# Kernel optimization log

Hardware: AMD Instinct MI355X
Metric: run time of the kernel (lower is better)

## Reference

```python
import jax, jax.numpy as jnp
import numpy as np

V = 100000   # nodes
E = 1600000  # edges (avg degree 16)
LN = 64      # feat_dim
S = 8        # stat_dim
T = 4        # recurrence steps
MU = 0.9
N_EDGE_TYPES = 10


def _uniform_linear(kw, kb, fan_out, fan_in):
    # torch nn.Linear default init: U(-1/sqrt(fan_in), 1/sqrt(fan_in))
    lim = 1.0 / np.sqrt(fan_in)
    W = jax.random.uniform(kw, (fan_out, fan_in), jnp.float32, -lim, lim)
    b = jax.random.uniform(kb, (fan_out,), jnp.float32, -lim, lim)
    return W, b


def setup_inputs() -> dict:
    key = jax.random.key(0)
    ks = jax.random.split(key, 12)
    feat_Matrix = jax.random.normal(ks[0], (V, LN), jnp.float32)
    X_Node = jax.random.randint(ks[1], (E,), 1, V + 1, dtype=jnp.int64)   # 1-indexed
    X_Neis = jax.random.randint(ks[2], (E,), 1, V + 1, dtype=jnp.int64)   # 1-indexed
    edge_type_index = jax.random.randint(ks[3], (E,), 1, N_EDGE_TYPES + 1, dtype=jnp.int32)
    dg_list = jax.random.randint(ks[4], (E,), 1, 65).astype(jnp.float32)  # degrees >= 1
    H_init = jax.random.uniform(ks[5], (V, S), jnp.float32)  # torch.rand init of state
    W_xi, b_xi = _uniform_linear(ks[6], ks[7], S * S, 2 * LN + N_EDGE_TYPES)
    W_rou, b_rou = _uniform_linear(ks[8], ks[9], S, LN)
    W1, b1 = _uniform_linear(ks[10], ks[11], 1, S)
    return {
        "feat_Matrix": feat_Matrix, "X_Node": X_Node, "X_Neis": X_Neis,
        "edge_type_index": edge_type_index, "dg_list": dg_list, "H_init": H_init,
        "W_xi": W_xi, "b_xi": b_xi, "W_rou": W_rou, "b_rou": b_rou,
        "W1": W1, "b1": b1,
    }


def reference(feat_Matrix, X_Node, X_Neis, edge_type_index, dg_list, H_init,
              W_xi, b_xi, W_rou, b_rou, W1, b1):
    src = X_Node - 1           # 0-indexed source nodes
    dst = X_Neis - 1           # 0-indexed neighbor nodes (for embedding gather)
    node_emb = feat_Matrix[src]            # [E, LN]
    neis_emb = feat_Matrix[dst]            # [E, LN]
    et = jax.nn.one_hot(edge_type_index - 1, N_EDGE_TYPES, dtype=jnp.float32)
    X = jnp.concatenate([node_emb, neis_emb, et], axis=1)  # [E, 2*LN+10]

    # Xi(X): per-edge transition matrices A, constant across steps -> precompute
    A = jnp.tanh(X @ W_xi.T + b_xi).reshape(-1, S, S)
    A = A * (MU / S) / dg_list[:, None, None]              # [E, S, S]
    # Rou(neis_emb): per-edge bias b, constant across steps
    bias = jnp.tanh(neis_emb @ W_rou.T + b_rou)            # [E, S]

    def step(H, _):
        He = H[src]                                        # gather [E, S]
        out = jnp.einsum('eij,ej->ei', A, He) + bias       # per-edge small matmul
        # AggrSum: dense one-hot mask vs RAW 1-indexed X_Neis against range(0,V-1)
        # -> scatter by 1-indexed ids; ids == V fall out of range and are dropped.
        Hn = jax.ops.segment_sum(out, X_Neis, num_segments=V)
        return Hn, None

    H, _ = jax.lax.scan(step, H_init, None, length=T)      # [V, S]

    logits = (H @ W1.T + b1).squeeze(-1)                   # [V]
    attn = jax.nn.softmax(logits)                          # softmax over nodes
    graph_out = jnp.tanh(jnp.sum(H * attn[:, None], axis=0))  # [S]
    return graph_out
```

## Files before the change

kernel.cpp:

```cpp
#include <hip/hip_runtime.h>
#include <hip/hip_bf16.h>

constexpr int V   = 100000;
constexpr int E   = 1600000;
constexpr int NET = 10;
constexpr int KXW = 138;
constexpr int NB  = (V + 255) / 256;
constexpr int GN  = 8;
constexpr float MUS   = 0.1125f;
constexpr float SP    = 0.025f;
constexpr float LOG2E = 1.44269504f;
constexpr float S2L   = 2.0f * SP * LOG2E;
constexpr float K7    = MUS / 7.0f;

typedef __attribute__((ext_vector_type(8))) short short8;
typedef __attribute__((ext_vector_type(4))) float float4v;

__device__ __forceinline__ float fast_tanh(float x) {
    return 1.0f - 2.0f * __builtin_amdgcn_rcpf(__expf(2.0f * x) + 1.0f);
}
__device__ __forceinline__ float bflo(unsigned u) { return __uint_as_float(u << 16); }
__device__ __forceinline__ float bfhi(unsigned u) { return __uint_as_float(u & 0xffff0000u); }
__device__ __forceinline__ short f2bf(float x) {
    union { __hip_bfloat16 b; short s; } u; u.b = __float2bfloat16(x); return u.s;
}

__device__ __forceinline__ float ub0(unsigned u) {
#if __has_builtin(__builtin_amdgcn_cvt_f32_ubyte0)
    return __builtin_amdgcn_cvt_f32_ubyte0(u);
#else
    return (float)(u & 0xff);
#endif
}
__device__ __forceinline__ float ub1(unsigned u) {
#if __has_builtin(__builtin_amdgcn_cvt_f32_ubyte1)
    return __builtin_amdgcn_cvt_f32_ubyte1(u);
#else
    return (float)((u >> 8) & 0xff);
#endif
}
__device__ __forceinline__ float ub2(unsigned u) {
#if __has_builtin(__builtin_amdgcn_cvt_f32_ubyte2)
    return __builtin_amdgcn_cvt_f32_ubyte2(u);
#else
    return (float)((u >> 16) & 0xff);
#endif
}
__device__ __forceinline__ float ub3(unsigned u) {
#if __has_builtin(__builtin_amdgcn_cvt_f32_ubyte3)
    return __builtin_amdgcn_cvt_f32_ubyte3(u);
#else
    return (float)(u >> 24);
#endif
}

__device__ __forceinline__ int dot8i4(unsigned a, unsigned b, int c) {
#if __has_builtin(__builtin_amdgcn_sdot8)
    return __builtin_amdgcn_sdot8((int)a, (int)b, c, false);
#else
    int r = c;
    #pragma unroll
    for (int j = 0; j < 8; ++j) {
        int av = ((int)(a << (28 - 4 * j))) >> 28;
        int bv = ((int)(b << (28 - 4 * j))) >> 28;
        r += av * bv;
    }
    return r;
#endif
}

__global__ __launch_bounds__(256) void histg_kernel(
    const int* __restrict__ xneis, int* __restrict__ countg,
    int* __restrict__ rank0)
{
    int e = blockIdx.x * 256 + threadIdx.x;
    if (e >= E) return;
    int g = blockIdx.x & (GN - 1);
    int nr = xneis[e];
    if (nr < V) rank0[e] = atomicAdd(&countg[g * V + nr], 1);
}

__global__ __launch_bounds__(256) void scanV_kernel(
    const int* __restrict__ countg, int* __restrict__ offg,
    int* __restrict__ cnt_tot, int* __restrict__ scanned, int* __restrict__ bsum)
{
    __shared__ int s[256];
    int tid = threadIdx.x;
    int i = blockIdx.x * 256 + tid;
    int c = 0;
    if (i < V) {
        int run = 0;
        #pragma unroll
        for (int g = 0; g < GN; ++g) {
            offg[g * V + i] = run;
            run += countg[g * V + i];
        }
        cnt_tot[i] = run;
        c = run;
    }
    s[tid] = c; __syncthreads();
    #pragma unroll
    for (int off = 1; off < 256; off <<= 1) {
        int t = (tid >= off) ? s[tid - off] : 0;
        __syncthreads();
        s[tid] += t;
        __syncthreads();
    }
    if (i < V) scanned[i] = s[tid] - c;
    if (tid == 255) bsum[blockIdx.x] = s[255];
}

__global__ __launch_bounds__(512) void scan_tops_kernel(
    const int* __restrict__ blocksum, int* __restrict__ tops, int* __restrict__ rowptr)
{
    __shared__ int s[512];
    int tid = threadIdx.x;
    int v = (tid < NB) ? blocksum[tid] : 0;
    s[tid] = v; __syncthreads();
    #pragma unroll
    for (int off = 1; off < 512; off <<= 1) {
        int t = (tid >= off) ? s[tid - off] : 0;
        __syncthreads();
        s[tid] += t;
        __syncthreads();
    }
    if (tid < NB) tops[tid] = s[tid] - v;
    if (tid == 511) rowptr[V] = s[511];
}

__global__ __launch_bounds__(256) void add_offsets_kernel(
    const int* __restrict__ scanned, const int* __restrict__ tops, int* __restrict__ rowptr)
{
    int i = blockIdx.x * 256 + threadIdx.x;
    if (i < V) rowptr[i] = scanned[i] + tops[blockIdx.x];
}

__global__ __launch_bounds__(256) void scatter_kernel(
    const int* __restrict__ xnode, const int* __restrict__ xneis,
    const int* __restrict__ etype, const float* __restrict__ dg,
    const int* __restrict__ rowptr, const int* __restrict__ offg,
    const int* __restrict__ rank0, unsigned* __restrict__ pmeta)
{
    int e = blockIdx.x * 256 + threadIdx.x;
    if (e >= E) return;
    int g = blockIdx.x & (GN - 1);
    int nr = xneis[e];
    if (nr < V) {
        int p = rowptr[nr] + offg[g * V + nr] + rank0[e];
        unsigned src = (unsigned)(xnode[e] - 1);
        unsigned et  = (unsigned)(etype[e] - 1);
        unsigned dgi = (unsigned)dg[e] - 1;
        pmeta[p] = src | (et << 17) | (dgi << 21);
    }
}

__global__ __launch_bounds__(256) void bsum_kernel(
    const float* __restrict__ feat, const int* __restrict__ count,
    const float* __restrict__ Wrou, const float* __restrict__ brou,
    const float* __restrict__ Hinit, float* __restrict__ Bsum,
    uint2* __restrict__ Hq0)
{
    __shared__ float Wl[512];
    __shared__ float bl[8];
    int tid = threadIdx.x;
    for (int i = tid; i < 512; i += 256) Wl[i] = Wrou[i];
    if (tid < 8) bl[tid] = brou[tid];
    __syncthreads();

    int v = blockIdx.x * 256 + tid;
    if (v >= V) return;
    int c = count[v];
    float out[8] = {0, 0, 0, 0, 0, 0, 0, 0};
    if (c > 0) {
        const float4* f4 = (const float4*)(feat + (size_t)(v - 1) * 64);
        float acc[8];
        #pragma unroll
        for (int s = 0; s < 8; ++s) acc[s] = bl[s];
        #pragma unroll 4
        for (int k = 0; k < 16; ++k) {
            float4 x = f4[k];
            #pragma unroll
            for (int s = 0; s < 8; ++s) {
                const float* w = &Wl[s * 64 + k * 4];
                acc[s] += x.x * w[0] + x.y * w[1] + x.z * w[2] + x.w * w[3];
            }
        }
        float fc = (float)c;
        #pragma unroll
        for (int s = 0; s < 8; ++s) out[s] = fc * fast_tanh(acc[s]);
    }
    float4* O = (float4*)(Bsum + (size_t)v * 8);
    O[0] = make_float4(out[0], out[1], out[2], out[3]);
    O[1] = make_float4(out[4], out[5], out[6], out[7]);

    const float4* Hh4 = (const float4*)(Hinit + (size_t)v * 8);
    float4 h0 = Hh4[0], h1 = Hh4[1];
    float hv[8] = {h0.x, h0.y, h0.z, h0.w, h1.x, h1.y, h1.z, h1.w};
    float mx = 0.0f;
    #pragma unroll
    for (int i = 0; i < 8; ++i) mx = fmaxf(mx, fabsf(hv[i]));
    float si = (mx > 0.0f) ? 7.0f / mx : 0.0f;
    unsigned w = 0;
    #pragma unroll
    for (int i = 0; i < 8; ++i)
        w |= ((unsigned)((int)rintf(hv[i] * si)) & 0xFu) << (4 * i);
    Hq0[v] = make_uint2(w, __float_as_uint(mx * (1.0f / 7.0f)));
}

__global__ __launch_bounds__(256) void pq_kernel(
    const float* __restrict__ feat, const float* __restrict__ Wxi,
    unsigned char* __restrict__ P8, ushort* __restrict__ Qb)
{
    const int lane = threadIdx.x & 63, wave = threadIdx.x >> 6;
    const int quad = lane >> 4, l16 = lane & 15;

    short8 bP[4][2], bQ[4][2];
    #pragma unroll
    for (int nt = 0; nt < 4; ++nt) {
        #pragma unroll
        for (int ks = 0; ks < 2; ++ks) {
            const float* wp = Wxi + (size_t)(nt * 16 + l16) * KXW + ks * 32 + quad * 8;
            short8 p, q;
            #pragma unroll
            for (int j = 0; j < 8; ++j) { p[j] = f2bf(wp[j]); q[j] = f2bf(wp[64 + j]); }
            bP[nt][ks] = p; bQ[nt][ks] = q;
        }
    }

    int t = blockIdx.x * 4 + wave;
    if (t >= V / 16) return;
    int v0 = t * 16;

    const float* fp = feat + (size_t)(v0 + l16) * 64 + quad * 8;
    short8 a0, a1;
    #pragma unroll
    for (int j = 0; j < 8; ++j) { a0[j] = f2bf(fp[j]); a1[j] = f2bf(fp[32 + j]); }

    float4v accP[4], accQ[4];
    #pragma unroll
    for (int nt = 0; nt < 4; ++nt) {
        float4v z = {0.f, 0.f, 0.f, 0.f};
        z = __builtin_amdgcn_mfma_f32_16x16x32_bf16(a0, bP[nt][0], z, 0, 0, 0);
        z = __builtin_amdgcn_mfma_f32_16x16x32_bf16(a1, bP[nt][1], z, 0, 0, 0);
        accP[nt] = z;
        float4v w = {0.f, 0.f, 0.f, 0.f};
        w = __builtin_amdgcn_mfma_f32_16x16x32_bf16(a0, bQ[nt][0], w, 0, 0, 0);
        w = __builtin_amdgcn_mfma_f32_16x16x32_bf16(a1, bQ[nt][1], w, 0, 0, 0);
        accQ[nt] = w;
    }

    #pragma unroll
    for (int r = 0; r < 4; ++r) {
        int row = v0 + quad * 4 + r;
        #pragma unroll
        for (int nt = 0; nt < 4; ++nt) {
            int col = nt * 16 + l16;
            int q8 = (int)rintf(accP[nt][r] * (1.0f / SP)) + 128;
            q8 = min(max(q8, 0), 255);
            P8[row * 64 + col] = (unsigned char)q8;
            Qb[row * 64 + col] = (ushort)f2bf(accQ[nt][r]);
        }
    }
}

__global__ __launch_bounds__(256) void amat_kernel(
    const unsigned* __restrict__ pmeta, const int* __restrict__ rowptr,
    const unsigned char* __restrict__ P8, const ushort* __restrict__ Qb,
    const float* __restrict__ Wxi, const float* __restrict__ bxi,
    const uint2* __restrict__ Hq0, const float* __restrict__ Bsum,
    unsigned* __restrict__ A4, uint2* __restrict__ HqOut)
{
    __shared__ float Wet2[NET * 64];
    int tid = threadIdx.x;
    for (int i = tid; i < NET * 64; i += 256) {
        int et = i >> 6, n = i & 63;
        Wet2[i] = 2.0f * LOG2E * (Wxi[n * KXW + 128 + et] + bxi[n]);
    }
    __syncthreads();

    int v = blockIdx.x * 4 + (tid >> 6);
    if (v >= V) return;
    int lane = tid & 63;
    int el = lane >> 3, s = lane & 7;

    const int off = rowptr[v];
    const int deg = rowptr[v + 1] - off;

    float q0, q1, q2, q3, q4, q5, q6, q7;
    {
        uint4 qu = *(const uint4*)(Qb + v * 64 + s * 8);
        const float B = 128.0f * SP, C = 2.0f * LOG2E;
        q0 = C * (bflo(qu.x) - B); q1 = C * (bfhi(qu.x) - B);
        q2 = C * (bflo(qu.y) - B); q3 = C * (bfhi(qu.y) - B);
        q4 = C * (bflo(qu.z) - B); q5 = C * (bfhi(qu.z) - B);
        q6 = C * (bflo(qu.w) - B); q7 = C * (bfhi(qu.w) - B);
    }

    float accD = 0.0f;

    for (int base = 0; base < deg; base += 64) {
        unsigned m_mine = 0;
        {
            int i1 = base + lane;
            if (i1 < deg) m_mine = pmeta[off + i1];
        }
        int nb = deg - base;
        for (int k = 0; k * 8 + el < nb && k < 8; ++k) {
            int ib = k * 8 + el;
            int i = base + ib;
            unsigned m = __shfl(m_mine, ib);
            int src = (int)(m & 0x1FFFF);
            int et  = (int)((m >> 17) & 0xF);

            uint2 pu = *(const uint2*)(P8 + src * 64 + s * 8);
            const float4* w4 = (const float4*)(&Wet2[et * 64 + s * 8]);
            float4 wa = w4[0], wb = w4[1];
            uint2 hq = Hq0[src];

            float r0 = __builtin_amdgcn_rcpf(__builtin_amdgcn_exp2f(fmaf(ub0(pu.x), S2L, q0 + wa.x)) + 1.0f);
            float r1 = __builtin_amdgcn_rcpf(__builtin_amdgcn_exp2f(fmaf(ub1(pu.x), S2L, q1 + wa.y)) + 1.0f);
            float r2 = __builtin_amdgcn_rcpf(__builtin_amdgcn_exp2f(fmaf(ub2(pu.x), S2L, q2 + wa.z)) + 1.0f);
            float r3 = __builtin_amdgcn_rcpf(__builtin_amdgcn_exp2f(fmaf(ub3(pu.x), S2L, q3 + wa.w)) + 1.0f);
            float r4 = __builtin_amdgcn_rcpf(__builtin_amdgcn_exp2f(fmaf(ub0(pu.y), S2L, q4 + wb.x)) + 1.0f);
            float r5 = __builtin_amdgcn_rcpf(__builtin_amdgcn_exp2f(fmaf(ub1(pu.y), S2L, q5 + wb.y)) + 1.0f);
            float r6 = __builtin_amdgcn_rcpf(__builtin_amdgcn_exp2f(fmaf(ub2(pu.y), S2L, q6 + wb.z)) + 1.0f);
            float r7 = __builtin_amdgcn_rcpf(__builtin_amdgcn_exp2f(fmaf(ub3(pu.y), S2L, q7 + wb.w)) + 1.0f);

            int n0 = (int)rintf(fmaf(r0, -14.0f, 7.0f));
            int n1 = (int)rintf(fmaf(r1, -14.0f, 7.0f));
            int n2 = (int)rintf(fmaf(r2, -14.0f, 7.0f));
            int n3 = (int)rintf(fmaf(r3, -14.0f, 7.0f));
            int n4 = (int)rintf(fmaf(r4, -14.0f, 7.0f));
            int n5 = (int)rintf(fmaf(r5, -14.0f, 7.0f));
            int n6 = (int)rintf(fmaf(r6, -14.0f, 7.0f));
            int n7 = (int)rintf(fmaf(r7, -14.0f, 7.0f));

            unsigned w = ((unsigned)n0 & 0xFu)        | (((unsigned)n1 & 0xFu) << 4)
                       | (((unsigned)n2 & 0xFu) << 8)  | (((unsigned)n3 & 0xFu) << 12)
                       | (((unsigned)n4 & 0xFu) << 16) | (((unsigned)n5 & 0xFu) << 20)
                       | (((unsigned)n6 & 0xFu) << 24) | (((unsigned)n7 & 0xFu) << 28);
            A4[(unsigned)(off + i) * 8u + (unsigned)s] = w;

            int dd = dot8i4(w, hq.x, 0);
            float rdg = __builtin_amdgcn_rcpf((float)((int)(m >> 21) + 1));
            accD = fmaf((float)dd, __uint_as_float(hq.y) * rdg, accD);
        }
    }
    accD += __shfl_xor(accD, 8);  accD += __shfl_xor(accD, 16); accD += __shfl_xor(accD, 32);
    float h1v = accD * K7 + Bsum[v * 8 + s];

    float mx = fabsf(h1v);
    mx = fmaxf(mx, __shfl_xor(mx, 1));
    mx = fmaxf(mx, __shfl_xor(mx, 2));
    mx = fmaxf(mx, __shfl_xor(mx, 4));
    float si = (mx > 0.0f) ? 7.0f / mx : 0.0f;
    unsigned nib = (unsigned)((int)rintf(h1v * si)) & 0xFu;
    unsigned b1 = __shfl(nib, lane + 1), b2 = __shfl(nib, lane + 2), b3 = __shfl(nib, lane + 3);
    unsigned b4 = __shfl(nib, lane + 4), b5 = __shfl(nib, lane + 5);
    unsigned b6 = __shfl(nib, lane + 6), b7 = __shfl(nib, lane + 7);
    if (lane == 0) {
        unsigned w = nib | (b1 << 4) | (b2 << 8) | (b3 << 12)
                   | (b4 << 16) | (b5 << 20) | (b6 << 24) | (b7 << 28);
        HqOut[v] = make_uint2(w, __float_as_uint(mx * (1.0f / 7.0f)));
    }
}

__global__ __launch_bounds__(256) void step_kernel(
    const uint2* __restrict__ HqIn, uint2* __restrict__ HqOut,
    const unsigned* __restrict__ pmeta, const int* __restrict__ rowptr,
    const unsigned* __restrict__ A4, const float* __restrict__ Bsum,
    const float* __restrict__ W1, const float* __restrict__ b1,
    float* __restrict__ logitsOut, float* __restrict__ HfpOut)
{
    int v = blockIdx.x * 64 + (threadIdx.x >> 2);
    if (v >= V) return;
    int q = threadIdx.x & 3;

    int p0 = rowptr[v], p1 = rowptr[v + 1];

    float accE = 0.0f, accO = 0.0f;
    for (int p = p0; p < p1; ++p) {
        unsigned m = pmeta[p];
        int src = (int)(m & 0x1FFFFu);
        uint2 au = *(const uint2*)(A4 + (unsigned)p * 8u + (unsigned)(q * 2));
        uint2 hq = HqIn[src];
        int dE = dot8i4(au.x, hq.x, 0);
        int dO = dot8i4(au.y, hq.x, 0);
        float rdg = __builtin_amdgcn_rcpf((float)((int)(m >> 21) + 1));
        float sc = __uint_as_float(hq.y) * rdg;
        accE = fmaf((float)dE, sc, accE);
        accO = fmaf((float)dO, sc, accO);
    }

    float hE = accE * K7 + Bsum[v * 8 + q * 2];
    float hO = accO * K7 + Bsum[v * 8 + q * 2 + 1];

    float mx = fmaxf(fabsf(hE), fabsf(hO));
    mx = fmaxf(mx, __shfl_xor(mx, 1));
    mx = fmaxf(mx, __shfl_xor(mx, 2));
    float si = (mx > 0.0f) ? 7.0f / mx : 0.0f;
    unsigned nE = (unsigned)((int)rintf(hE * si)) & 0xFu;
    unsigned nO = (unsigned)((int)rintf(hO * si)) & 0xFu;
    unsigned wq = (nE | (nO << 4)) << (8 * q);
    wq |= __shfl_xor(wq, 1);
    wq |= __shfl_xor(wq, 2);
    if (q == 0)
        HqOut[v] = make_uint2(wq, __float_as_uint(mx * (1.0f / 7.0f)));
    if (HfpOut != nullptr)
        *(float2*)(HfpOut + v * 8 + q * 2) = make_float2(hE, hO);
    if (logitsOut != nullptr) {
        float t = hE * W1[q * 2] + hO * W1[q * 2 + 1];
        t += __shfl_xor(t, 1); t += __shfl_xor(t, 2);
        if (q == 0) logitsOut[v] = t + b1[0];
    }
}

__global__ __launch_bounds__(256) void reduce_max_kernel(
    const float* __restrict__ logits, float* __restrict__ partial)
{
    float m = -INFINITY;
    for (int v = blockIdx.x * 256 + threadIdx.x; v < V; v += 256 * 256)
        m = fmaxf(m, logits[v]);
    #pragma unroll
    for (int o = 32; o > 0; o >>= 1) m = fmaxf(m, __shfl_down(m, o));
    __shared__ float sm[4];
    if ((threadIdx.x & 63) == 0) sm[threadIdx.x >> 6] = m;
    __syncthreads();
    if (threadIdx.x == 0)
        partial[blockIdx.x] = fmaxf(fmaxf(sm[0], sm[1]), fmaxf(sm[2], sm[3]));
}

__global__ __launch_bounds__(256) void final_max_kernel(
    const float* __restrict__ partial, float* __restrict__ M)
{
    float m = partial[threadIdx.x];
    #pragma unroll
    for (int o = 32; o > 0; o >>= 1) m = fmaxf(m, __shfl_down(m, o));
    __shared__ float sm[4];
    if ((threadIdx.x & 63) == 0) sm[threadIdx.x >> 6] = m;
    __syncthreads();
    if (threadIdx.x == 0) *M = fmaxf(fmaxf(sm[0], sm[1]), fmaxf(sm[2], sm[3]));
}

__global__ __launch_bounds__(256) void sum_kernel(
    const float* __restrict__ H, const float* __restrict__ logits,
    const float* __restrict__ Mp, float* __restrict__ partial)
{
    const float M = *Mp;
    float se = 0.0f;
    float sh[8] = {0, 0, 0, 0, 0, 0, 0, 0};
    for (int v = blockIdx.x * 256 + threadIdx.x; v < V; v += 64 * 256) {
        float w = __expf(logits[v] - M);
        se += w;
        const float4* H4 = (const float4*)(H + (size_t)v * 8);
        float4 h0 = H4[0], h1 = H4[1];
        sh[0] += w * h0.x; sh[1] += w * h0.y; sh[2] += w * h0.z; sh[3] += w * h0.w;
        sh[4] += w * h1.x; sh[5] += w * h1.y; sh[6] += w * h1.z; sh[7] += w * h1.w;
    }
    #pragma unroll
    for (int o = 32; o > 0; o >>= 1) {
        se += __shfl_xor(se, o);
        #pragma unroll
        for (int i = 0; i < 8; ++i) sh[i] += __shfl_xor(sh[i], o);
    }
    __shared__ float sm[4][9];
    int wv = threadIdx.x >> 6;
    if ((threadIdx.x & 63) == 0) {
        sm[wv][8] = se;
        #pragma unroll
        for (int i = 0; i < 8; ++i) sm[wv][i] = sh[i];
    }
    __syncthreads();
    if (threadIdx.x == 0) {
        #pragma unroll
        for (int i = 0; i < 9; ++i)
            partial[blockIdx.x * 12 + i] = sm[0][i] + sm[1][i] + sm[2][i] + sm[3][i];
    }
}

__global__ void final_kernel(const float* __restrict__ partial, float* __restrict__ out)
{
    int lane = threadIdx.x;
    float vals[9];
    #pragma unroll
    for (int i = 0; i < 9; ++i) vals[i] = partial[lane * 12 + i];
    #pragma unroll
    for (int o = 1; o < 64; o <<= 1) {
        #pragma unroll
        for (int i = 0; i < 9; ++i) vals[i] += __shfl_xor(vals[i], o);
    }
    __shared__ float res[9];
    if (lane == 0) {
        #pragma unroll
        for (int i = 0; i < 9; ++i) res[i] = vals[i];
    }
    __syncthreads();
    if (lane < 8) out[lane] = tanhf(res[lane] / res[8]);
}

extern "C" void kernel_launch(void* const* d_in, const int* in_sizes, int n_in,
                              void* d_out, int out_size, void* d_ws, size_t ws_size,
                              hipStream_t stream)
{
    const float* feat  = (const float*)d_in[0];
    const int*   xnode = (const int*)d_in[1];
    const int*   xneis = (const int*)d_in[2];
    const int*   etype = (const int*)d_in[3];
    const float* dg    = (const float*)d_in[4];
    const float* Hinit = (const float*)d_in[5];
    const float* Wxi   = (const float*)d_in[6];
    const float* bxi   = (const float*)d_in[7];
    const float* Wrou  = (const float*)d_in[8];
    const float* brou  = (const float*)d_in[9];
    const float* W1    = (const float*)d_in[10];
    const float* b1    = (const float*)d_in[11];

    char* ws = (char*)d_ws;
    auto alloc = [&](size_t bytes) -> char* {
        char* p = ws; ws += (bytes + 255) & ~(size_t)255; return p;
    };
    unsigned* A4      = (unsigned*)alloc((size_t)E * 32);
    unsigned char* P8 = (unsigned char*)alloc((size_t)V * 64);
    ushort*   Qb      = (ushort*)alloc((size_t)V * 64 * 2);
    unsigned* pmeta   = (unsigned*)alloc((size_t)E * 4);
    int*      rank0   = (int*)alloc((size_t)E * 4);
    int*      countg  = (int*)alloc((size_t)GN * V * 4);
    int*      offg    = (int*)alloc((size_t)GN * V * 4);
    int*      cnt     = (int*)alloc((size_t)V * 4);
    int*      scanned = (int*)alloc((size_t)V * 4);
    int*      rowptr  = (int*)alloc((size_t)(V + 1) * 4);
    int*      bsumT   = (int*)alloc(512 * 4);
    int*      topsT   = (int*)alloc(512 * 4);
    uint2*    Hq0     = (uint2*)alloc((size_t)V * 8);
    uint2*    HqA     = (uint2*)alloc((size_t)V * 8);
    uint2*    HqB     = (uint2*)alloc((size_t)V * 8);
    float*    Hfp     = (float*)alloc((size_t)V * 8 * 4);
    float*    Bsum    = (float*)alloc((size_t)V * 8 * 4);
    float*    logits  = (float*)alloc((size_t)V * 4);
    float*    pmax    = (float*)alloc(256 * 4);
    float*    Mp      = (float*)alloc(16);
    float*    spart   = (float*)alloc(64 * 12 * 4);

    hipMemsetAsync(countg, 0, (size_t)GN * V * 4, stream);
    histg_kernel<<<(E + 255) / 256, 256, 0, stream>>>(xneis, countg, rank0);
    scanV_kernel<<<NB, 256, 0, stream>>>(countg, offg, cnt, scanned, bsumT);
    scan_tops_kernel<<<1, 512, 0, stream>>>(bsumT, topsT, rowptr);
    add_offsets_kernel<<<NB, 256, 0, stream>>>(scanned, topsT, rowptr);
    scatter_kernel<<<(E + 255) / 256, 256, 0, stream>>>(xnode, xneis, etype, dg,
                                                        rowptr, offg, rank0, pmeta);
    pq_kernel<<<(V / 16 + 3) / 4, 256, 0, stream>>>(feat, Wxi, P8, Qb);
    bsum_kernel<<<NB, 256, 0, stream>>>(feat, cnt, Wrou, brou, Hinit,
                                        Bsum, Hq0);
    amat_kernel<<<(V + 3) / 4, 256, 0, stream>>>(pmeta, rowptr, P8, Qb, Wxi, bxi,
                                                 Hq0, Bsum, A4, HqA);

    const uint2* Hcur = HqA;
    uint2* bufs[2] = {HqB, HqA};
    for (int t = 0; t < 3; ++t) {
        uint2* Hn = bufs[t & 1];
        float* lg  = (t == 2) ? logits : nullptr;
        float* hf  = (t == 2) ? Hfp : nullptr;
        step_kernel<<<(V + 63) / 64, 256, 0, stream>>>(Hcur, Hn, pmeta, rowptr,
                                                       A4, Bsum, W1, b1, lg, hf);
        Hcur = Hn;
    }

    reduce_max_kernel<<<256, 256, 0, stream>>>(logits, pmax);
    final_max_kernel<<<1, 256, 0, stream>>>(pmax, Mp);
    sum_kernel<<<64, 256, 0, stream>>>(Hfp, logits, Mp, spart);
    final_kernel<<<1, 64, 0, stream>>>(spart, (float*)d_out);
}
```

Before: 430.1 us.

## Split CSR scatter into radix-bucketed staging pass and per-range drain kernel

The direct random scatter of edge metadata into CSR order is replaced by two passes. First, each block buckets its edges by the high bits of the destination position into 8 ranges using wave ballots, writing (position, meta) pairs contiguously. A drain kernel then handles one range per block group, so its writes land in a 1 MB window of pmeta that should stay cache-resident. This adds an extra kernel launch plus roughly 26 MB of staging traffic in exchange for better write locality.

```diff
diff --git a/kernel.cpp b/kernel.cpp
--- a/kernel.cpp
+++ b/kernel.cpp
@@ -7,6 +7,7 @@
 constexpr int KXW = 138;
 constexpr int NB  = (V + 255) / 256;
 constexpr int GN  = 8;
+constexpr int NEB = E / 256;
 constexpr float MUS   = 0.1125f;
 constexpr float SP    = 0.025f;
 constexpr float LOG2E = 1.44269504f;
@@ -135,22 +136,68 @@
     if (i < V) rowptr[i] = scanned[i] + tops[blockIdx.x];
 }
 
-__global__ __launch_bounds__(256) void scatter_kernel(
+__global__ __launch_bounds__(256) void scatterA_kernel(
     const int* __restrict__ xnode, const int* __restrict__ xneis,
     const int* __restrict__ etype, const float* __restrict__ dg,
     const int* __restrict__ rowptr, const int* __restrict__ offg,
-    const int* __restrict__ rank0, unsigned* __restrict__ pmeta)
-{
-    int e = blockIdx.x * 256 + threadIdx.x;
-    if (e >= E) return;
+    const int* __restrict__ rank0, uint2* __restrict__ buc,
+    int* __restrict__ bcnt)
+{
+    __shared__ int wcnt[4][8];
+    __shared__ int woff[4][8];
+    int tid = threadIdx.x;
+    int lane = tid & 63, wv = tid >> 6;
+    int e = blockIdx.x * 256 + tid;
     int g = blockIdx.x & (GN - 1);
+
     int nr = xneis[e];
-    if (nr < V) {
-        int p = rowptr[nr] + offg[g * V + nr] + rank0[e];
+    bool keep = (nr < V);
+    int p = -1, r = 0;
+    if (keep) {
+        p = rowptr[nr] + offg[g * V + nr] + rank0[e];
+        r = p >> 18;
+    }
+
+    unsigned rnk = 0;
+    #pragma unroll
+    for (int r8 = 0; r8 < 8; ++r8) {
+        unsigned long long m = __ballot(keep && (r == r8));
+        if (keep && r == r8)
+            rnk = (unsigned)__popcll(m & ((1ull << lane) - 1ull));
+        if (lane == 0) wcnt[wv][r8] = (int)__popcll(m);
+    }
+    __syncthreads();
+    if (tid < 8) {
+        int run = 0;
+        #pragma unroll
+        for (int w = 0; w < 4; ++w) { woff[w][tid] = run; run += wcnt[w][tid]; }
+        bcnt[blockIdx.x * 8 + tid] = run;
+    }
+    __syncthreads();
+
+    if (keep) {
         unsigned src = (unsigned)(xnode[e] - 1);
         unsigned et  = (unsigned)(etype[e] - 1);
         unsigned dgi = (unsigned)dg[e] - 1;
-        pmeta[p] = src | (et << 17) | (dgi << 21);
+        unsigned meta = src | (et << 17) | (dgi << 21);
+        int slot = blockIdx.x * 2048 + r * 256 + woff[wv][r] + (int)rnk;
+        buc[slot] = make_uint2((unsigned)p, meta);
+    }
+}
+
+__global__ __launch_bounds__(256) void drain_kernel(
+    const uint2* __restrict__ buc, const int* __restrict__ bcnt,
+    unsigned* __restrict__ pmeta)
+{
+    int r = blockIdx.x & 7;
+    int nstride = (int)(gridDim.x >> 3);
+    for (int sb = (int)(blockIdx.x >> 3); sb < NEB; sb += nstride) {
+        int c = bcnt[sb * 8 + r];
+        const uint2* seg = buc + (size_t)sb * 2048 + r * 256;
+        for (int i = threadIdx.x; i < c; i += 256) {
+            uint2 t = seg[i];
+            pmeta[t.x] = t.y;
+        }
     }
 }
 
@@ -520,12 +567,14 @@
         char* p = ws; ws += (bytes + 255) & ~(size_t)255; return p;
     };
     unsigned* A4      = (unsigned*)alloc((size_t)E * 32);
+    uint2*    buc     = (uint2*)alloc((size_t)NEB * 2048 * 8);
     unsigned char* P8 = (unsigned char*)alloc((size_t)V * 64);
     ushort*   Qb      = (ushort*)alloc((size_t)V * 64 * 2);
     unsigned* pmeta   = (unsigned*)alloc((size_t)E * 4);
     int*      rank0   = (int*)alloc((size_t)E * 4);
     int*      countg  = (int*)alloc((size_t)GN * V * 4);
     int*      offg    = (int*)alloc((size_t)GN * V * 4);
+    int*      bcnt    = (int*)alloc((size_t)NEB * 8 * 4);
     int*      cnt     = (int*)alloc((size_t)V * 4);
     int*      scanned = (int*)alloc((size_t)V * 4);
     int*      rowptr  = (int*)alloc((size_t)(V + 1) * 4);
@@ -542,12 +591,13 @@
     float*    spart   = (float*)alloc(64 * 12 * 4);
 
     hipMemsetAsync(countg, 0, (size_t)GN * V * 4, stream);
-    histg_kernel<<<(E + 255) / 256, 256, 0, stream>>>(xneis, countg, rank0);
+    histg_kernel<<<NEB, 256, 0, stream>>>(xneis, countg, rank0);
     scanV_kernel<<<NB, 256, 0, stream>>>(countg, offg, cnt, scanned, bsumT);
     scan_tops_kernel<<<1, 512, 0, stream>>>(bsumT, topsT, rowptr);
     add_offsets_kernel<<<NB, 256, 0, stream>>>(scanned, topsT, rowptr);
-    scatter_kernel<<<(E + 255) / 256, 256, 0, stream>>>(xnode, xneis, etype, dg,
-                                                        rowptr, offg, rank0, pmeta);
+    scatterA_kernel<<<NEB, 256, 0, stream>>>(xnode, xneis, etype, dg,
+                                             rowptr, offg, rank0, buc, bcnt);
+    drain_kernel<<<2048, 256, 0, stream>>>(buc, bcnt, pmeta);
     pq_kernel<<<(V / 16 + 3) / 4, 256, 0, stream>>>(feat, Wxi, P8, Qb);
     bsum_kernel<<<NB, 256, 0, stream>>>(feat, cnt, Wrou, brou, Hinit,
                                         Bsum, Hq0);
```

Measured after the change: 427.7 us. Within noise of the previous version (-0.6%).
